# Optimization experiments

Hardware: AMD Instinct MI355X
Metric: run time of the kernel (lower is better)

## Reference

```python
import jax, jax.numpy as jnp
import numpy as np

B, H, W, A, C = 8, 13, 13, 5, 20
ANCHORS = [[1.3221, 1.73145], [3.19275, 4.00944], [5.05587, 8.09892],
           [9.47112, 4.84053], [11.2364, 10.0071]]
L_COORD, OBJ_SCALE, NOOBJ_SCALE = 3.0, 5.0, 1.0
POS_FRAC_THRESH = 0.98


def gen_yolo_box():
    # anchor[..., 0:2] = (x_col, y_row) grid offsets, anchor[..., 2:4] = anchor (w, h)
    ys, xs = jnp.meshgrid(jnp.arange(H, dtype=jnp.float32),
                          jnp.arange(W, dtype=jnp.float32), indexing='ij')
    grid = jnp.broadcast_to(jnp.stack([xs, ys], -1)[:, :, None, :], (H, W, A, 2))
    wh = jnp.broadcast_to(jnp.asarray(ANCHORS, jnp.float32)[None, None], (H, W, A, 2))
    return jnp.concatenate([grid, wh], -1)  # [H, W, A, 4]


def decode(delta, anc, fs0, fs1):
    # delta: [..., 4] raw offsets; anc: [..., 4]; returns [x1, y1, w, h]
    w = jnp.exp(delta[..., 2]) * anc[..., 2] / fs0
    h = jnp.exp(delta[..., 3]) * anc[..., 3] / fs1
    x = (delta[..., 0] + anc[..., 0]) / fs0 - w * 0.5
    y = (delta[..., 1] + anc[..., 1]) / fs1 - h * 0.5
    return jnp.stack([x, y, w, h], -1)


def pairwise_iou(b1, b2):
    # b1: [N,4], b2: [M,4] in [x1,y1,w,h]; returns [N, M]
    b1x1, b1y1 = b1[:, 0:1], b1[:, 1:2]
    b1x2, b1y2 = b1x1 + b1[:, 2:3], b1y1 + b1[:, 3:4]
    b2x1, b2y1, b2x2, b2y2 = b2[:, 0], b2[:, 1], b2[:, 0] + b2[:, 2], b2[:, 1] + b2[:, 3]
    dx = jnp.clip(jnp.minimum(b1x2, b2x2[None, :]) - jnp.maximum(b1x1, b2x1[None, :]), 0)
    dy = jnp.clip(jnp.minimum(b1y2, b2y2[None, :]) - jnp.maximum(b1y1, b2y1[None, :]), 0)
    inter = dx * dy
    a1 = (b1x2 - b1x1) * (b1y2 - b1y1)          # [N,1]
    a2 = (b2x2 - b2x1) * (b2y2 - b2y1)          # [M]
    return inter / (a1 + a2[None, :] - inter)


def elem_iou(b1, b2):
    # elementwise IoU over [..., 4] boxes ([x1,y1,w,h])
    b1x2, b1y2 = b1[..., 0] + b1[..., 2], b1[..., 1] + b1[..., 3]
    b2x2, b2y2 = b2[..., 0] + b2[..., 2], b2[..., 1] + b2[..., 3]
    dx = jnp.clip(jnp.minimum(b1x2, b2x2) - jnp.maximum(b1[..., 0], b2[..., 0]), 0)
    dy = jnp.clip(jnp.minimum(b1y2, b2y2) - jnp.maximum(b1[..., 1], b2[..., 1]), 0)
    inter = dx * dy
    a1 = b1[..., 2] * b1[..., 3]
    a2 = b2[..., 2] * b2[..., 3]
    return inter / (a1 + a2 - inter)


def setup_inputs() -> dict:
    key = jax.random.key(0)
    ks = jax.random.split(key, 6)
    pred_cls = jax.random.normal(ks[0], (B, H, W, A, C), jnp.float32)
    pred_conf = jax.random.uniform(ks[1], (B, H, W, A, 1), jnp.float32)
    pred_bboxes = jax.random.normal(ks[2], (B, H, W, A, 4), jnp.float32)
    label_cls = jax.random.normal(ks[3], (B, H, W, A, C), jnp.float32)
    u = jax.random.uniform(ks[4], (B, H, W, A, 1), jnp.float32)
    label_conf = (u > POS_FRAC_THRESH).astype(jnp.float32)  # sparse positives
    label_bboxes = jax.random.uniform(ks[5], (B, H, W, A, 4), jnp.float32)
    return {"pred_cls": pred_cls, "pred_conf": pred_conf, "pred_bboxes": pred_bboxes,
            "label_cls": label_cls, "label_conf": label_conf, "label_bboxes": label_bboxes}


def reference(pred_cls, pred_conf, pred_bboxes, label_cls, label_conf, label_bboxes):
    dt = pred_bboxes.dtype
    fs0, fs1 = float(H), float(W)
    pos = label_conf[..., 0] > 0                 # [B,H,W,A]
    posf = pos.astype(dt)
    anc = gen_yolo_box()[None]                   # [1,H,W,A,4]

    gt_box = decode(label_bboxes, anc, fs0, fs1)   # [B,H,W,A,4]
    pred_box = decode(pred_bboxes, anc, fs0, fs1)  # [B,H,W,A,4]

    # "diagonal" IoU: each positive gt paired with the pred box at the same cell
    diag_iou = elem_iou(gt_box, pred_box)          # [B,H,W,A]
    p_conf = pred_conf[..., 0]
    loss_pos_conf = jnp.sum(posf * (p_conf - jax.lax.stop_gradient(diag_iou)) ** 2) \
        * OBJ_SCALE / B

    # dense masked pairwise IoU (gt rows masked to 0 where not positive)
    N = B * H * W * A
    iou_mat = pairwise_iou(gt_box.reshape(N, 4), pred_box.reshape(N, 4))  # [N,N]
    pos_flat = pos.reshape(N)
    iou_mat = jnp.where(pos_flat[:, None], iou_mat, jnp.zeros((), dt))
    best = jnp.max(iou_mat, axis=0)                       # per pred box
    best = jnp.where(pos_flat, jnp.ones((), dt), best)    # ious_[pos] = 1
    negf = (best < 0.6).astype(dt)
    loss_neg_conf = jnp.sum(negf * (p_conf.reshape(N) - label_conf.reshape(N)) ** 2) \
        * NOOBJ_SCALE / B

    # classification CE (sum) over positives
    logp = jax.nn.log_softmax(pred_cls, axis=-1)
    lbl = jnp.argmax(label_cls, axis=-1)
    nll = -jnp.take_along_axis(logp, lbl[..., None], axis=-1)[..., 0]
    loss_cls = jnp.sum(posf * nll) / B

    # coordinate losses over positives
    dxy = pred_bboxes[..., :2] - label_bboxes[..., :2]
    loss_x = jnp.sum(posf * dxy[..., 0] ** 2) * L_COORD / B
    loss_y = jnp.sum(posf * dxy[..., 1] ** 2) * L_COORD / B

    def huber(d):  # SmoothL1, beta=1
        ad = jnp.abs(d)
        return jnp.where(ad < 1.0, 0.5 * d * d, ad - 0.5)

    dwh = pred_bboxes[..., 2:4] - label_bboxes[..., 2:4]
    loss_w = jnp.sum(posf * huber(dwh[..., 0])) * L_COORD / B
    loss_h = jnp.sum(posf * huber(dwh[..., 1])) * L_COORD / B

    return loss_x + loss_y + loss_w + loss_h + loss_cls + loss_neg_conf + loss_pos_conf
```

## Files before the change

### kernel.cpp

```cpp
#include <hip/hip_runtime.h>

#define NB 8
#define HH 13
#define WW 13
#define AA 5
#define CC 20
#define NTOT (NB * HH * WW * AA)
#define L_COORD 3.0f
#define OBJ_SCALE 5.0f
#define NOOBJ_SCALE 1.0f
#define INV_B (1.0f / 8.0f)
#define FS 13.0f
#define CHUNK 1024

__device__ __constant__ float c_anc[AA][2] = {
    {1.3221f, 1.73145f}, {3.19275f, 4.00944f}, {5.05587f, 8.09892f},
    {9.47112f, 4.84053f}, {11.2364f, 10.0071f}};

__device__ __forceinline__ float block_reduce_sum(float v, float* sbuf) {
    for (int o = 32; o > 0; o >>= 1) v += __shfl_down(v, o);
    int lane = threadIdx.x & 63;
    int wid  = threadIdx.x >> 6;
    if (lane == 0) sbuf[wid] = v;
    __syncthreads();
    float s = 0.f;
    if (threadIdx.x == 0) {
        int nw = (blockDim.x + 63) >> 6;
        for (int i = 0; i < nw; i++) s += sbuf[i];
    }
    return s;
}

__global__ void __launch_bounds__(256) yolo_fused_kernel(
    const float* __restrict__ pred_cls,
    const float* __restrict__ pred_conf,
    const float* __restrict__ pred_bboxes,
    const float* __restrict__ label_cls,
    const float* __restrict__ label_conf,
    const float* __restrict__ label_bboxes,
    float* __restrict__ out) {
    __shared__ float sgx1[CHUNK], sgy1[CHUNK], sgx2[CHUNK], sgy2[CHUNK], sgar[CHUNK];
    __shared__ int s_cnt;
    __shared__ float sred[4];

    const int tid = threadIdx.x;
    const int n   = blockIdx.x * blockDim.x + tid;

    float local = 0.f;
    bool  neg   = false;
    float px1 = 0.f, py1 = 0.f, px2 = 0.f, py2 = 0.f, parea = 1.f, diffsq = 0.f;

    if (n < NTOT) {
        int a = n % AA;
        int w = (n / AA) % WW;
        int h = (n / (AA * WW)) % HH;
        float ancx = (float)w, ancy = (float)h;
        float ancw = c_anc[a][0], anch = c_anc[a][1];

        float p0 = pred_bboxes[n * 4 + 0];
        float p1 = pred_bboxes[n * 4 + 1];
        float p2 = pred_bboxes[n * 4 + 2];
        float p3 = pred_bboxes[n * 4 + 3];
        float pw = expf(p2) * ancw / FS;
        float ph = expf(p3) * anch / FS;
        px1 = (p0 + ancx) / FS - pw * 0.5f;
        py1 = (p1 + ancy) / FS - ph * 0.5f;
        px2 = px1 + pw;
        py2 = py1 + ph;
        parea = pw * ph;

        float lcf = label_conf[n];
        float pc  = pred_conf[n];
        if (lcf > 0.f) {
            float t0 = label_bboxes[n * 4 + 0];
            float t1 = label_bboxes[n * 4 + 1];
            float t2 = label_bboxes[n * 4 + 2];
            float t3 = label_bboxes[n * 4 + 3];
            float gw = expf(t2) * ancw / FS;
            float gh = expf(t3) * anch / FS;
            float gx = (t0 + ancx) / FS - gw * 0.5f;
            float gy = (t1 + ancy) / FS - gh * 0.5f;
            float gx2 = gx + gw, gy2 = gy + gh;

            float dx = fminf(gx2, px2) - fmaxf(gx, px1); dx = fmaxf(dx, 0.f);
            float dy = fminf(gy2, py2) - fmaxf(gy, py1); dy = fmaxf(dy, 0.f);
            float inter = dx * dy;
            float iou = inter / (gw * gh + parea - inter);

            float dconf = pc - iou;
            local += OBJ_SCALE * dconf * dconf;

            const float* lc   = label_cls + (long)n * CC;
            const float* pcls = pred_cls + (long)n * CC;
            int lbl = 0;
            float bl = lc[0];
            for (int i = 1; i < CC; i++) {
                float v = lc[i];
                if (v > bl) { bl = v; lbl = i; }
            }
            float mx = pcls[0];
            for (int i = 1; i < CC; i++) mx = fmaxf(mx, pcls[i]);
            float s = 0.f;
            for (int i = 0; i < CC; i++) s += expf(pcls[i] - mx);
            local += mx + logf(s) - pcls[lbl];

            float dxc = p0 - t0, dyc = p1 - t1;
            local += L_COORD * (dxc * dxc + dyc * dyc);
            float dwc = p2 - t2, dhc = p3 - t3;
            float adw = fabsf(dwc), adh = fabsf(dhc);
            float hw  = adw < 1.f ? 0.5f * dwc * dwc : adw - 0.5f;
            float hh2 = adh < 1.f ? 0.5f * dhc * dhc : adh - 0.5f;
            local += L_COORD * (hw + hh2);
        } else {
            neg = true;
            float d = pc - lcf;
            diffsq = d * d;
        }
    }

    float best = 0.f;
    for (int base = 0; base < NTOT; base += CHUNK) {
        if (tid == 0) s_cnt = 0;
        __syncthreads();
        int lim = min(base + CHUNK, NTOT);
        for (int c = base + tid; c < lim; c += 256) {
            if (label_conf[c] > 0.f) {
                int a = c % AA;
                int w = (c / AA) % WW;
                int h = (c / (AA * WW)) % HH;
                float t0 = label_bboxes[c * 4 + 0];
                float t1 = label_bboxes[c * 4 + 1];
                float t2 = label_bboxes[c * 4 + 2];
                float t3 = label_bboxes[c * 4 + 3];
                float gw = expf(t2) * c_anc[a][0] / FS;
                float gh = expf(t3) * c_anc[a][1] / FS;
                float gx = (t0 + (float)w) / FS - gw * 0.5f;
                float gy = (t1 + (float)h) / FS - gh * 0.5f;
                int idx = atomicAdd(&s_cnt, 1);
                sgx1[idx] = gx;
                sgy1[idx] = gy;
                sgx2[idx] = gx + gw;
                sgy2[idx] = gy + gh;
                sgar[idx] = gw * gh;
            }
        }
        __syncthreads();
        int m = s_cnt;
        if (neg) {
            for (int i = 0; i < m; i++) {
                float dx = fminf(px2, sgx2[i]) - fmaxf(px1, sgx1[i]);
                dx = fmaxf(dx, 0.f);
                float dy = fminf(py2, sgy2[i]) - fmaxf(py1, sgy1[i]);
                dy = fmaxf(dy, 0.f);
                float inter = dx * dy;
                float iou = inter / (sgar[i] + parea - inter);
                best = fmaxf(best, iou);
            }
        }
        __syncthreads();
    }

    if (neg && best < 0.6f) local += diffsq;

    float bs = block_reduce_sum(local, sred);
    if (tid == 0) atomicAdd(out, bs * INV_B);
}

extern "C" void kernel_launch(void* const* d_in, const int* in_sizes, int n_in,
                              void* d_out, int out_size, void* d_ws, size_t ws_size,
                              hipStream_t stream) {
    const float* pred_cls     = (const float*)d_in[0];
    const float* pred_conf    = (const float*)d_in[1];
    const float* pred_bboxes  = (const float*)d_in[2];
    const float* label_cls    = (const float*)d_in[3];
    const float* label_conf   = (const float*)d_in[4];
    const float* label_bboxes = (const float*)d_in[5];
    float* out = (float*)d_out;

    const int block = 256;
    const int grid  = (NTOT + block - 1) / block;

    yolo_fused_kernel<<<grid, block, 0, stream>>>(
        pred_cls, pred_conf, pred_bboxes, label_cls, label_conf, label_bboxes, out);
}
```

Before: 103.4 us.

## Vectorize box/class loads and enlarge gt chunk to cut sync rounds

```diff
diff --git a/kernel.cpp b/kernel.cpp
--- a/kernel.cpp
+++ b/kernel.cpp
@@ -8,10 +8,13 @@
 #define NTOT (NB * HH * WW * AA)
 #define L_COORD 3.0f
 #define OBJ_SCALE 5.0f
-#define NOOBJ_SCALE 1.0f
 #define INV_B (1.0f / 8.0f)
 #define FS 13.0f
-#define CHUNK 1024
+#define BLOCK 256
+#define GRID ((NTOT + BLOCK - 1) / BLOCK)
+#define CAP 4064
+#define NCHUNK ((NTOT + CAP - 1) / CAP)
+#define MAXITER 16
 
 __device__ __constant__ float c_anc[AA][2] = {
     {1.3221f, 1.73145f}, {3.19275f, 4.00944f}, {5.05587f, 8.09892f},
@@ -19,32 +22,29 @@
 
 __device__ __forceinline__ float block_reduce_sum(float v, float* sbuf) {
     for (int o = 32; o > 0; o >>= 1) v += __shfl_down(v, o);
-    int lane = threadIdx.x & 63;
-    int wid  = threadIdx.x >> 6;
-    if (lane == 0) sbuf[wid] = v;
+    if ((threadIdx.x & 63) == 0) sbuf[threadIdx.x >> 6] = v;
     __syncthreads();
     float s = 0.f;
     if (threadIdx.x == 0) {
-        int nw = (blockDim.x + 63) >> 6;
-        for (int i = 0; i < nw; i++) s += sbuf[i];
+        for (int i = 0; i < (BLOCK >> 6); i++) s += sbuf[i];
     }
     return s;
 }
 
-__global__ void __launch_bounds__(256) yolo_fused_kernel(
+__global__ void __launch_bounds__(BLOCK) yolo_fused_kernel(
     const float* __restrict__ pred_cls,
     const float* __restrict__ pred_conf,
-    const float* __restrict__ pred_bboxes,
+    const float4* __restrict__ pred_bboxes,
     const float* __restrict__ label_cls,
     const float* __restrict__ label_conf,
-    const float* __restrict__ label_bboxes,
+    const float4* __restrict__ label_bboxes,
     float* __restrict__ out) {
-    __shared__ float sgx1[CHUNK], sgy1[CHUNK], sgx2[CHUNK], sgy2[CHUNK], sgar[CHUNK];
+    __shared__ float4 sbox[CAP];
     __shared__ int s_cnt;
-    __shared__ float sred[4];
+    __shared__ float sred[BLOCK >> 6];
 
     const int tid = threadIdx.x;
-    const int n   = blockIdx.x * blockDim.x + tid;
+    const int n   = blockIdx.x * BLOCK + tid;
 
     float local = 0.f;
     bool  neg   = false;
@@ -54,32 +54,26 @@
         int a = n % AA;
         int w = (n / AA) % WW;
         int h = (n / (AA * WW)) % HH;
-        float ancx = (float)w, ancy = (float)h;
         float ancw = c_anc[a][0], anch = c_anc[a][1];
 
-        float p0 = pred_bboxes[n * 4 + 0];
-        float p1 = pred_bboxes[n * 4 + 1];
-        float p2 = pred_bboxes[n * 4 + 2];
-        float p3 = pred_bboxes[n * 4 + 3];
-        float pw = expf(p2) * ancw / FS;
-        float ph = expf(p3) * anch / FS;
-        px1 = (p0 + ancx) / FS - pw * 0.5f;
-        py1 = (p1 + ancy) / FS - ph * 0.5f;
+        float4 pb  = pred_bboxes[n];
+        float  lcf = label_conf[n];
+        float  pc  = pred_conf[n];
+
+        float pw = expf(pb.z) * ancw * (1.f / FS);
+        float ph = expf(pb.w) * anch * (1.f / FS);
+        px1 = (pb.x + (float)w) * (1.f / FS) - pw * 0.5f;
+        py1 = (pb.y + (float)h) * (1.f / FS) - ph * 0.5f;
         px2 = px1 + pw;
         py2 = py1 + ph;
         parea = pw * ph;
 
-        float lcf = label_conf[n];
-        float pc  = pred_conf[n];
         if (lcf > 0.f) {
-            float t0 = label_bboxes[n * 4 + 0];
-            float t1 = label_bboxes[n * 4 + 1];
-            float t2 = label_bboxes[n * 4 + 2];
-            float t3 = label_bboxes[n * 4 + 3];
-            float gw = expf(t2) * ancw / FS;
-            float gh = expf(t3) * anch / FS;
-            float gx = (t0 + ancx) / FS - gw * 0.5f;
-            float gy = (t1 + ancy) / FS - gh * 0.5f;
+            float4 tb = label_bboxes[n];
+            float gw = expf(tb.z) * ancw * (1.f / FS);
+            float gh = expf(tb.w) * anch * (1.f / FS);
+            float gx = (tb.x + (float)w) * (1.f / FS) - gw * 0.5f;
+            float gy = (tb.y + (float)h) * (1.f / FS) - gh * 0.5f;
             float gx2 = gx + gw, gy2 = gy + gh;
 
             float dx = fminf(gx2, px2) - fmaxf(gx, px1); dx = fmaxf(dx, 0.f);
@@ -90,23 +84,35 @@
             float dconf = pc - iou;
             local += OBJ_SCALE * dconf * dconf;
 
-            const float* lc   = label_cls + (long)n * CC;
-            const float* pcls = pred_cls + (long)n * CC;
+            const float4* lc4 = reinterpret_cast<const float4*>(label_cls) + (long)n * 5;
+            const float4* pc4 = reinterpret_cast<const float4*>(pred_cls) + (long)n * 5;
+            float lrow[CC], prow[CC];
+            #pragma unroll
+            for (int q = 0; q < 5; q++) {
+                float4 v = lc4[q];
+                lrow[4 * q + 0] = v.x; lrow[4 * q + 1] = v.y;
+                lrow[4 * q + 2] = v.z; lrow[4 * q + 3] = v.w;
+                float4 u = pc4[q];
+                prow[4 * q + 0] = u.x; prow[4 * q + 1] = u.y;
+                prow[4 * q + 2] = u.z; prow[4 * q + 3] = u.w;
+            }
             int lbl = 0;
-            float bl = lc[0];
+            float bl = lrow[0];
+            #pragma unroll
             for (int i = 1; i < CC; i++) {
-                float v = lc[i];
-                if (v > bl) { bl = v; lbl = i; }
+                if (lrow[i] > bl) { bl = lrow[i]; lbl = i; }
             }
-            float mx = pcls[0];
-            for (int i = 1; i < CC; i++) mx = fmaxf(mx, pcls[i]);
+            float mx = prow[0];
+            #pragma unroll
+            for (int i = 1; i < CC; i++) mx = fmaxf(mx, prow[i]);
             float s = 0.f;
-            for (int i = 0; i < CC; i++) s += expf(pcls[i] - mx);
-            local += mx + logf(s) - pcls[lbl];
+            #pragma unroll
+            for (int i = 0; i < CC; i++) s += expf(prow[i] - mx);
+            local += mx + logf(s) - prow[lbl];
 
-            float dxc = p0 - t0, dyc = p1 - t1;
+            float dxc = pb.x - tb.x, dyc = pb.y - tb.y;
             local += L_COORD * (dxc * dxc + dyc * dyc);
-            float dwc = p2 - t2, dhc = p3 - t3;
+            float dwc = pb.z - tb.z, dhc = pb.w - tb.w;
             float adw = fabsf(dwc), adh = fabsf(dhc);
             float hw  = adw < 1.f ? 0.5f * dwc * dwc : adw - 0.5f;
             float hh2 = adh < 1.f ? 0.5f * dhc * dhc : adh - 0.5f;
@@ -119,41 +125,47 @@
     }
 
     float best = 0.f;
-    for (int base = 0; base < NTOT; base += CHUNK) {
+    for (int chunk = 0; chunk < NCHUNK; ++chunk) {
+        const int base = chunk * CAP;
+        const int rem  = min(CAP, NTOT - base);
+
+        float cv[MAXITER];
+        #pragma unroll
+        for (int k = 0; k < MAXITER; k++) {
+            int idx = tid + (k << 8);
+            cv[k] = (idx < rem) ? label_conf[base + idx] : 0.f;
+        }
         if (tid == 0) s_cnt = 0;
         __syncthreads();
-        int lim = min(base + CHUNK, NTOT);
-        for (int c = base + tid; c < lim; c += 256) {
-            if (label_conf[c] > 0.f) {
+
+        #pragma unroll
+        for (int k = 0; k < MAXITER; k++) {
+            int idx = tid + (k << 8);
+            if (idx < rem && cv[k] > 0.f) {
+                int c = base + idx;
                 int a = c % AA;
                 int w = (c / AA) % WW;
                 int h = (c / (AA * WW)) % HH;
-                float t0 = label_bboxes[c * 4 + 0];
-                float t1 = label_bboxes[c * 4 + 1];
-                float t2 = label_bboxes[c * 4 + 2];
-                float t3 = label_bboxes[c * 4 + 3];
-                float gw = expf(t2) * c_anc[a][0] / FS;
-                float gh = expf(t3) * c_anc[a][1] / FS;
-                float gx = (t0 + (float)w) / FS - gw * 0.5f;
-                float gy = (t1 + (float)h) / FS - gh * 0.5f;
-                int idx = atomicAdd(&s_cnt, 1);
-                sgx1[idx] = gx;
-                sgy1[idx] = gy;
-                sgx2[idx] = gx + gw;
-                sgy2[idx] = gy + gh;
-                sgar[idx] = gw * gh;
+                float4 tb = label_bboxes[c];
+                float gw = expf(tb.z) * c_anc[a][0] * (1.f / FS);
+                float gh = expf(tb.w) * c_anc[a][1] * (1.f / FS);
+                float gx = (tb.x + (float)w) * (1.f / FS) - gw * 0.5f;
+                float gy = (tb.y + (float)h) * (1.f / FS) - gh * 0.5f;
+                int s = atomicAdd(&s_cnt, 1);
+                sbox[s] = make_float4(gx, gy, gx + gw, gy + gh);
             }
         }
         __syncthreads();
-        int m = s_cnt;
+        const int m = s_cnt;
         if (neg) {
+            #pragma unroll 4
             for (int i = 0; i < m; i++) {
-                float dx = fminf(px2, sgx2[i]) - fmaxf(px1, sgx1[i]);
-                dx = fmaxf(dx, 0.f);
-                float dy = fminf(py2, sgy2[i]) - fmaxf(py1, sgy1[i]);
-                dy = fmaxf(dy, 0.f);
+                float4 g = sbox[i];
+                float dx = fminf(px2, g.z) - fmaxf(px1, g.x); dx = fmaxf(dx, 0.f);
+                float dy = fminf(py2, g.w) - fmaxf(py1, g.y); dy = fmaxf(dy, 0.f);
                 float inter = dx * dy;
-                float iou = inter / (sgar[i] + parea - inter);
+                float garea = (g.z - g.x) * (g.w - g.y);
+                float iou = inter / (garea + parea - inter);
                 best = fmaxf(best, iou);
             }
         }
@@ -169,17 +181,14 @@
 extern "C" void kernel_launch(void* const* d_in, const int* in_sizes, int n_in,
                               void* d_out, int out_size, void* d_ws, size_t ws_size,
                               hipStream_t stream) {
-    const float* pred_cls     = (const float*)d_in[0];
-    const float* pred_conf    = (const float*)d_in[1];
-    const float* pred_bboxes  = (const float*)d_in[2];
-    const float* label_cls    = (const float*)d_in[3];
-    const float* label_conf   = (const float*)d_in[4];
-    const float* label_bboxes = (const float*)d_in[5];
+    const float*  pred_cls     = (const float*)d_in[0];
+    const float*  pred_conf    = (const float*)d_in[1];
+    const float4* pred_bboxes  = (const float4*)d_in[2];
+    const float*  label_cls    = (const float*)d_in[3];
+    const float*  label_conf   = (const float*)d_in[4];
+    const float4* label_bboxes = (const float4*)d_in[5];
     float* out = (float*)d_out;
 
-    const int block = 256;
-    const int grid  = (NTOT + block - 1) / block;
-
-    yolo_fused_kernel<<<grid, block, 0, stream>>>(
+    yolo_fused_kernel<<<GRID, BLOCK, 0, stream>>>(
         pred_cls, pred_conf, pred_bboxes, label_cls, label_conf, label_bboxes, out);
 }
```

Result: faster. 95.72 us (-7.4%).
